# Kernel optimization log

Measured on AMD Instinct MI355X. Metric: run time of the kernel, lower is better.

The kernel has to match this reference:

```python
import jax, jax.numpy as jnp
import numpy as np

N = 8192      # number of points
K = 64        # max_num_neighbors in radius()
C_IN = 64     # input feature channels
R = 0.125     # radius r


def setup_inputs() -> dict:
    key = jax.random.key(0)
    ks = jax.random.split(key, 8)
    s = 0.05
    return {
        "x": jax.random.normal(ks[0], (N, C_IN), jnp.float32),
        "pos": jax.random.uniform(ks[1], (N, 3), jnp.float32),
        "batch": jnp.zeros((N,), jnp.int32),
        "W1": jax.random.normal(ks[2], (C_IN + 3, 64), jnp.float32) * s,
        "b1": jnp.zeros((64,), jnp.float32),
        "W2": jax.random.normal(ks[3], (64, 128), jnp.float32) * s,
        "b2": jnp.zeros((128,), jnp.float32),
        "Wg": jax.random.normal(ks[4], (128, 256), jnp.float32) * s,
        "bg": jnp.zeros((256,), jnp.float32),
    }


def reference(x, pos, batch, W1, b1, W2, b2, Wg, bg):
    # --- radius neighbor search (K nearest within radius R, self included) ---
    sq = jnp.sum(pos * pos, axis=-1)                     # [N]
    d2 = sq[:, None] + sq[None, :] - 2.0 * (pos @ pos.T)  # [N, N] squared dists
    same = batch[:, None] == batch[None, :]
    d2 = jnp.where(same, d2, jnp.inf)
    neg_d2, idx = jax.lax.top_k(-d2, K)                  # [N, K] nearest K per target
    valid = (-neg_d2) <= R * R                           # within-radius mask; self always valid

    # --- PointConv message: feature_nn(concat(x_j, pos_j - pos_i)) ---
    rel = pos[idx] - pos[:, None, :]                     # [N, K, 3]
    feat = jnp.concatenate([x[idx], rel], axis=-1)       # [N, K, C_IN+3]
    h = jax.nn.relu(feat @ W1 + b1)                      # [N, K, 64]
    h = jax.nn.relu(h @ W2 + b2)                         # [N, K, 128]

    # --- max aggregation over neighbors ---
    h = jnp.where(valid[..., None], h, -jnp.inf)
    agg = jnp.max(h, axis=1)                             # [N, 128]

    # --- global_nn ---
    out = jax.nn.relu(agg @ Wg + bg)                     # [N, 256]
    return out
```

## Files before the change

kernel.cpp:

```cpp
#include <hip/hip_runtime.h>

#define N_PTS 8192
#define R2F 0.015625f

__global__ __launch_bounds__(256) void k_g(const float* __restrict__ x,
                                           const float* __restrict__ W1,
                                           float* __restrict__ g) {
    __shared__ float xs[32][68];
    __shared__ float ws_[64][64];
    const int t = threadIdx.x;
    const int r0 = blockIdx.x * 32;
    for (int v = t; v < 1024; v += 256)
        ((float4*)&ws_[0][0])[v] = ((const float4*)W1)[v];
    for (int v = t; v < 512; v += 256) {
        const int n = v >> 4, c4 = (v & 15) * 4;
        *(float4*)&xs[n][c4] = *(const float4*)&x[(r0 + n) * 64 + c4];
    }
    __syncthreads();
    const int c0 = (t & 15) * 4, n0 = (t >> 4) * 2;
    float acc[2][4];
    #pragma unroll
    for (int ni = 0; ni < 2; ++ni)
        #pragma unroll
        for (int ci = 0; ci < 4; ++ci) acc[ni][ci] = 0.0f;
    #pragma unroll
    for (int kb4 = 0; kb4 < 16; ++kb4) {
        float4 av[2], wv[4];
        #pragma unroll
        for (int ni = 0; ni < 2; ++ni)
            av[ni] = *(const float4*)&xs[n0 + ni][kb4 * 4];
        #pragma unroll
        for (int ki = 0; ki < 4; ++ki)
            wv[ki] = *(const float4*)&ws_[kb4 * 4 + ki][c0];
        #pragma unroll
        for (int ki = 0; ki < 4; ++ki) {
            #pragma unroll
            for (int ni = 0; ni < 2; ++ni) {
                const float a = (&av[ni].x)[ki];
                acc[ni][0] = __fmaf_rn(a, wv[ki].x, acc[ni][0]);
                acc[ni][1] = __fmaf_rn(a, wv[ki].y, acc[ni][1]);
                acc[ni][2] = __fmaf_rn(a, wv[ki].z, acc[ni][2]);
                acc[ni][3] = __fmaf_rn(a, wv[ki].w, acc[ni][3]);
            }
        }
    }
    #pragma unroll
    for (int ni = 0; ni < 2; ++ni)
        *(float4*)&g[(r0 + n0 + ni) * 64 + c0] =
            make_float4(acc[ni][0], acc[ni][1], acc[ni][2], acc[ni][3]);
}

__device__ __forceinline__ unsigned d2key(const float* __restrict__ pos, int j,
                                          float xi, float yi, float zi,
                                          float sqi) {
    const float xj = pos[j * 3 + 0], yj = pos[j * 3 + 1], zj = pos[j * 3 + 2];
    const float sqj = __fadd_rn(__fadd_rn(__fmul_rn(xj, xj), __fmul_rn(yj, yj)),
                                __fmul_rn(zj, zj));
    const float dot = __fmaf_rn(zi, zj, __fmaf_rn(yi, yj, __fmul_rn(xi, xj)));
    const float d2  = __fsub_rn(__fadd_rn(sqi, sqj), __fmul_rn(2.0f, dot));
    unsigned b = __float_as_uint(d2);
    return (b & 0x80000000u) ? ~b : (b | 0x80000000u);
}

__global__ __launch_bounds__(256, 6) void k_sel(const float* __restrict__ pos,
                                                float* __restrict__ out) {
    __shared__ unsigned mb[4][64];
    __shared__ unsigned mj[4][64];

    const int t    = threadIdx.x;
    const int lane = t & 63;
    const int w    = t >> 6;
    const int qb   = w << 11;
    const int i    = blockIdx.x;

    const float xi = pos[i * 3 + 0], yi = pos[i * 3 + 1], zi = pos[i * 3 + 2];
    const float sqi = __fadd_rn(__fadd_rn(__fmul_rn(xi, xi), __fmul_rn(yi, yi)),
                                __fmul_rn(zi, zi));

    unsigned m1b = 0xFFFFFFFFu, m2b = 0xFFFFFFFFu,
             m3b = 0xFFFFFFFFu, m4b = 0xFFFFFFFFu;
    int      m1j = 0x7FFFFFFF,  m2j = 0x7FFFFFFF,
             m3j = 0x7FFFFFFF,  m4j = 0x7FFFFFFF;
    #pragma unroll
    for (int k = 0; k < 32; ++k) {
        const int j = qb + lane + (k << 6);
        const unsigned b = d2key(pos, j, xi, yi, zi, sqi);
        if (b < m1b) {
            m4b = m3b; m4j = m3j; m3b = m2b; m3j = m2j;
            m2b = m1b; m2j = m1j; m1b = b;   m1j = j;
        } else if (b < m2b) {
            m4b = m3b; m4j = m3j; m3b = m2b; m3j = m2j;
            m2b = b;   m2j = j;
        } else if (b < m3b) {
            m4b = m3b; m4j = m3j; m3b = b;   m3j = j;
        } else if (b < m4b) {
            m4b = b;   m4j = j;
        }
    }

    mb[w][lane] = 0xFFFFFFFFu;
    mj[w][lane] = 0xFFFFFF00u | (unsigned)((w << 6) | lane);

    unsigned removed = 0u;
    int      level = 0;
    unsigned lb = m1b;
    int      lj = m1j;
    for (int s = 0; s < 64; ++s) {
        unsigned rb = lb;
        int      rj = lj;
        #pragma unroll
        for (int off = 32; off > 0; off >>= 1) {
            const unsigned ob = (unsigned)__shfl_down((int)rb, off);
            const int      oj = __shfl_down(rj, off);
            if (ob < rb || (ob == rb && oj < rj)) { rb = ob; rj = oj; }
        }
        const unsigned wb = (unsigned)__shfl((int)rb, 0);
        const int      wj = __shfl(rj, 0);
        const unsigned db = (wb & 0x80000000u) ? (wb ^ 0x80000000u) : ~wb;
        if (!(__uint_as_float(db) <= R2F)) break;
        if (lane == 0) { mb[w][s] = wb; mj[w][s] = (unsigned)wj; }
        if (lb == wb && lj == wj) {
            removed |= 1u << ((wj - qb - lane) >> 6);
            ++level;
            if      (level == 1) { lb = m2b; lj = m2j; }
            else if (level == 2) { lb = m3b; lj = m3j; }
            else if (level == 3) { lb = m4b; lj = m4j; }
            else {
                lb = 0xFFFFFFFFu; lj = 0x7FFFFFFF;
                #pragma unroll 4
                for (int k = 0; k < 32; ++k) {
                    if (!(removed & (1u << k))) {
                        const int jr = qb + lane + (k << 6);
                        const unsigned b = d2key(pos, jr, xi, yi, zi, sqi);
                        if (b < lb) { lb = b; lj = jr; }
                    }
                }
            }
        }
    }
    __syncthreads();

    {
        const int p = lane;
        const unsigned be = mb[w][p];
        const unsigned je = mj[w][p];
        int rank = p;
        #pragma unroll
        for (int d = 1; d < 4; ++d) {
            const int wp = (w + d) & 3;
            int lo = 0;
            #pragma unroll
            for (int st = 32; st > 0; st >>= 1) {
                const int idx = lo + st - 1;
                const unsigned ob = mb[wp][idx];
                const unsigned oj = mj[wp][idx];
                if (ob < be || (ob == be && oj < je)) lo += st;
            }
            {
                const unsigned ob = mb[wp][lo];
                const unsigned oj = mj[wp][lo];
                if (ob < be || (ob == be && oj < je)) lo += 1;
            }
            rank += lo;
        }
        if (rank < 64) {
            const unsigned db = (be & 0x80000000u) ? (be ^ 0x80000000u) : ~be;
            const bool ok = (__uint_as_float(db) <= R2F);
            ((ushort*)(out + (size_t)i * 256))[rank] =
                (ushort)((je & 8191u) | (ok ? 0x8000u : 0u));
        }
    }
}

__global__ __launch_bounds__(256, 6) void k_mlp(const float* __restrict__ g,
                                                const float* __restrict__ pos,
                                                const float* __restrict__ W1,
                                                const float* __restrict__ b1,
                                                const float* __restrict__ W2,
                                                const float* __restrict__ b2,
                                                const float* __restrict__ Wg,
                                                const float* __restrict__ bg,
                                                float* __restrict__ out) {
    __shared__ float gs[64][68];
    __shared__ float pmw[4][128];
    __shared__ float aggS[128];
    __shared__ int   selj[64];
    __shared__ int   nvalidS;

    const int t = threadIdx.x;
    const int w = t >> 6;
    const int i = blockIdx.x;

    const float xi = pos[i * 3 + 0], yi = pos[i * 3 + 1], zi = pos[i * 3 + 2];

    bool ok = false;
    if (t < 64) {
        const unsigned sv = ((const ushort*)(out + (size_t)i * 256))[t];
        selj[t] = (int)(sv & 8191u);
        ok = (sv & 0x8000u) != 0u;
    }
    __syncthreads();

    for (int v = t; v < 1024; v += 256) {
        const int n = v >> 4, c4 = (v & 15) * 4;
        *(float4*)&gs[n][c4] = *(const float4*)&g[selj[n] * 64 + c4];
    }
    {
        const unsigned long long vm = __ballot(ok);
        if (t == 0) nvalidS = __popcll(vm);
    }
    __syncthreads();
    const int nvalid = nvalidS;

    {
        const int c0 = (t & 15) * 4, n0 = (t >> 4) * 4;
        float rr[4][3];
        #pragma unroll
        for (int ni = 0; ni < 4; ++ni) {
            const int j = selj[n0 + ni];
            rr[ni][0] = pos[j * 3 + 0] - xi;
            rr[ni][1] = pos[j * 3 + 1] - yi;
            rr[ni][2] = pos[j * 3 + 2] - zi;
        }
        float w1b[3][4], bb[4];
        #pragma unroll
        for (int ci = 0; ci < 4; ++ci) {
            w1b[0][ci] = W1[4096 + c0 + ci];
            w1b[1][ci] = W1[4160 + c0 + ci];
            w1b[2][ci] = W1[4224 + c0 + ci];
            bb[ci]     = b1[c0 + ci];
        }
        #pragma unroll
        for (int ni = 0; ni < 4; ++ni) {
            const int n = n0 + ni;
            const float4 gv = *(const float4*)&gs[n][c0];
            float4 hv;
            #pragma unroll
            for (int ci = 0; ci < 4; ++ci) {
                float a = (&gv.x)[ci];
                a = __fmaf_rn(rr[ni][0], w1b[0][ci], a);
                a = __fmaf_rn(rr[ni][1], w1b[1][ci], a);
                a = __fmaf_rn(rr[ni][2], w1b[2][ci], a);
                a = fmaxf(a + bb[ci], 0.0f);
                (&hv.x)[ci] = (n < nvalid) ? a : 0.0f;
            }
            *(float4*)&gs[n][c0] = hv;
        }
    }
    __syncthreads();

    {
        const float (*h1)[68] = gs;
        const int c4 = (t & 15) * 4;
        const int nb = (t >> 4) * 4;
        #pragma unroll
        for (int half = 0; half < 2; ++half) {
            const int ch0 = half * 64 + c4;
            float acc[4][4];
            #pragma unroll
            for (int ni = 0; ni < 4; ++ni)
                #pragma unroll
                for (int k = 0; k < 4; ++k) acc[ni][k] = 0.0f;

            #pragma unroll 2
            for (int ccb = 0; ccb < 16; ++ccb) {
                #pragma unroll
                for (int pr = 0; pr < 2; ++pr) {
                    const int cc0 = ccb * 4 + pr * 2;
                    const float4 wt0 = *(const float4*)&W2[(cc0 + 0) * 128 + ch0];
                    const float4 wt1 = *(const float4*)&W2[(cc0 + 1) * 128 + ch0];
                    #pragma unroll
                    for (int ni = 0; ni < 4; ++ni) {
                        const float2 av = *(const float2*)&h1[nb + ni][cc0];
                        acc[ni][0] = __fmaf_rn(av.x, wt0.x, acc[ni][0]);
                        acc[ni][1] = __fmaf_rn(av.x, wt0.y, acc[ni][1]);
                        acc[ni][2] = __fmaf_rn(av.x, wt0.z, acc[ni][2]);
                        acc[ni][3] = __fmaf_rn(av.x, wt0.w, acc[ni][3]);
                        acc[ni][0] = __fmaf_rn(av.y, wt1.x, acc[ni][0]);
                        acc[ni][1] = __fmaf_rn(av.y, wt1.y, acc[ni][1]);
                        acc[ni][2] = __fmaf_rn(av.y, wt1.z, acc[ni][2]);
                        acc[ni][3] = __fmaf_rn(av.y, wt1.w, acc[ni][3]);
                    }
                }
            }
            float m4v[4];
            #pragma unroll
            for (int k = 0; k < 4; ++k) {
                const float bb = b2[ch0 + k];
                float mm = 0.0f;
                #pragma unroll
                for (int ni = 0; ni < 4; ++ni)
                    if (nb + ni < nvalid) mm = fmaxf(mm, acc[ni][k] + bb);
                m4v[k] = mm;
            }
            #pragma unroll
            for (int k = 0; k < 4; ++k) {
                float v = m4v[k];
                v = fmaxf(v, __shfl_down(v, 32));
                v = fmaxf(v, __shfl_down(v, 16));
                m4v[k] = v;
            }
            if ((t & 63) < 16) {
                #pragma unroll
                for (int k = 0; k < 4; ++k) pmw[w][ch0 + k] = m4v[k];
            }
        }
    }
    __syncthreads();

    if (t < 128)
        aggS[t] = fmaxf(fmaxf(pmw[0][t], pmw[1][t]),
                        fmaxf(pmw[2][t], pmw[3][t]));
    __syncthreads();

    {
        float acc = 0.0f;
        #pragma unroll 8
        for (int k = 0; k < 128; ++k)
            acc = __fmaf_rn(aggS[k], Wg[k * 256 + t], acc);
        out[i * 256 + t] = fmaxf(acc + bg[t], 0.0f);
    }
}

extern "C" void kernel_launch(void* const* d_in, const int* in_sizes, int n_in,
                              void* d_out, int out_size, void* d_ws, size_t ws_size,
                              hipStream_t stream) {
    const float* x   = (const float*)d_in[0];
    const float* pos = (const float*)d_in[1];
    const float* W1 = (const float*)d_in[3];
    const float* b1 = (const float*)d_in[4];
    const float* W2 = (const float*)d_in[5];
    const float* b2 = (const float*)d_in[6];
    const float* Wg = (const float*)d_in[7];
    const float* bg = (const float*)d_in[8];
    float* out = (float*)d_out;

    float* g = (float*)d_ws;

    k_g<<<N_PTS / 32, 256, 0, stream>>>(x, W1, g);
    k_sel<<<N_PTS, 256, 0, stream>>>(pos, out);
    k_mlp<<<N_PTS, 256, 0, stream>>>(g, pos, W1, b1, W2, b2, Wg, bg, out);
}
```

Before: 376.9 us.

## Extract two nearest neighbors per wave-reduction round in selection loop

Each lane now keeps its two best candidates, and the wavefront shuffle reduction merges top-2 pairs. Each iteration can commit two neighbors, roughly halving the number of serial reduction rounds. Wave-uniform results are broadcast with readfirstlane instead of a shuffle. In exchange, each reduction step does twice the shuffles and compares, and the per-lane cache now triggers the full rescan after three pops instead of four.

Measured after the change: 380.4 us. Within noise of the previous version (+0.9%).

```diff
diff --git a/kernel.cpp b/kernel.cpp
--- a/kernel.cpp
+++ b/kernel.cpp
@@ -60,6 +60,10 @@
     const float d2  = __fsub_rn(__fadd_rn(sqi, sqj), __fmul_rn(2.0f, dot));
     unsigned b = __float_as_uint(d2);
     return (b & 0x80000000u) ? ~b : (b | 0x80000000u);
+}
+
+__device__ __forceinline__ bool lexlt(unsigned ab, int aj, unsigned bb, int bj) {
+    return ab < bb || (ab == bb && aj < bj);
 }
 
 __global__ __launch_bounds__(256, 6) void k_sel(const float* __restrict__ pos,
@@ -103,40 +107,77 @@
 
     unsigned removed = 0u;
     int      level = 0;
-    unsigned lb = m1b;
-    int      lj = m1j;
-    for (int s = 0; s < 64; ++s) {
-        unsigned rb = lb;
-        int      rj = lj;
+    unsigned c1b = m1b, c2b = m2b;
+    int      c1j = m1j, c2j = m2j;
+    int s = 0;
+    while (s < 64) {
+        unsigned r1b = c1b, r2b = c2b;
+        int      r1j = c1j, r2j = c2j;
         #pragma unroll
         for (int off = 32; off > 0; off >>= 1) {
-            const unsigned ob = (unsigned)__shfl_down((int)rb, off);
-            const int      oj = __shfl_down(rj, off);
-            if (ob < rb || (ob == rb && oj < rj)) { rb = ob; rj = oj; }
-        }
-        const unsigned wb = (unsigned)__shfl((int)rb, 0);
-        const int      wj = __shfl(rj, 0);
-        const unsigned db = (wb & 0x80000000u) ? (wb ^ 0x80000000u) : ~wb;
-        if (!(__uint_as_float(db) <= R2F)) break;
-        if (lane == 0) { mb[w][s] = wb; mj[w][s] = (unsigned)wj; }
-        if (lb == wb && lj == wj) {
-            removed |= 1u << ((wj - qb - lane) >> 6);
-            ++level;
-            if      (level == 1) { lb = m2b; lj = m2j; }
-            else if (level == 2) { lb = m3b; lj = m3j; }
-            else if (level == 3) { lb = m4b; lj = m4j; }
+            const unsigned o1b = (unsigned)__shfl_down((int)r1b, off);
+            const int      o1j = __shfl_down(r1j, off);
+            const unsigned o2b = (unsigned)__shfl_down((int)r2b, off);
+            const int      o2j = __shfl_down(r2j, off);
+            if (lexlt(o1b, o1j, r1b, r1j)) {
+                if (lexlt(o2b, o2j, r1b, r1j)) { r2b = o2b; r2j = o2j; }
+                else                           { r2b = r1b; r2j = r1j; }
+                r1b = o1b; r1j = o1j;
+            } else {
+                if (lexlt(o1b, o1j, r2b, r2j)) { r2b = o1b; r2j = o1j; }
+            }
+        }
+        const unsigned w1b = (unsigned)__builtin_amdgcn_readfirstlane((int)r1b);
+        const int      w1j = __builtin_amdgcn_readfirstlane(r1j);
+        const unsigned w2b = (unsigned)__builtin_amdgcn_readfirstlane((int)r2b);
+        const int      w2j = __builtin_amdgcn_readfirstlane(r2j);
+
+        const unsigned d1 = (w1b & 0x80000000u) ? (w1b ^ 0x80000000u) : ~w1b;
+        if (!(__uint_as_float(d1) <= R2F)) break;
+        const unsigned d2 = (w2b & 0x80000000u) ? (w2b ^ 0x80000000u) : ~w2b;
+        const bool take2 = (__uint_as_float(d2) <= R2F) && (s + 1 < 64);
+
+        if (lane == 0) {
+            mb[w][s] = w1b; mj[w][s] = (unsigned)w1j;
+            if (take2) { mb[w][s + 1] = w2b; mj[w][s + 1] = (unsigned)w2j; }
+        }
+
+        int npop = 0;
+        if (c1b == w1b && c1j == w1j) {
+            removed |= 1u << ((c1j - qb - lane) >> 6);
+            ++npop;
+        }
+        if (take2) {
+            if (c1b == w2b && c1j == w2j) {
+                removed |= 1u << ((c1j - qb - lane) >> 6);
+                ++npop;
+            } else if (c2b == w2b && c2j == w2j) {
+                removed |= 1u << ((c2j - qb - lane) >> 6);
+                ++npop;
+            }
+        }
+        if (npop) {
+            level += npop;
+            if      (level == 1) { c1b = m2b; c1j = m2j; c2b = m3b; c2j = m3j; }
+            else if (level == 2) { c1b = m3b; c1j = m3j; c2b = m4b; c2j = m4j; }
             else {
-                lb = 0xFFFFFFFFu; lj = 0x7FFFFFFF;
+                c1b = 0xFFFFFFFFu; c1j = 0x7FFFFFFF;
+                c2b = 0xFFFFFFFFu; c2j = 0x7FFFFFFF;
                 #pragma unroll 4
                 for (int k = 0; k < 32; ++k) {
                     if (!(removed & (1u << k))) {
                         const int jr = qb + lane + (k << 6);
                         const unsigned b = d2key(pos, jr, xi, yi, zi, sqi);
-                        if (b < lb) { lb = b; lj = jr; }
+                        if (b < c1b) {
+                            c2b = c1b; c2j = c1j; c1b = b; c1j = jr;
+                        } else if (b < c2b) {
+                            c2b = b; c2j = jr;
+                        }
                     }
                 }
             }
         }
+        s += take2 ? 2 : 1;
     }
     __syncthreads();
 
```
